# Performance work log

Measured on AMD Instinct MI355X. Metric: run time of the kernel, lower is better.

## Reference

```python
import jax, jax.numpy as jnp
import numpy as np

GROUP_SIZE = 32

def setup_inputs() -> dict:
    key = jax.random.key(0)
    k_x, k_w, k_b, k_se, k_zp = jax.random.split(key, 5)
    B, S, IN_CH, OUT_CH = 4, 2048, 4096, 4096
    n_groups = IN_CH // GROUP_SIZE
    x = jax.random.normal(k_x, (B, S, IN_CH), dtype=jnp.float32)
    weight = jax.random.normal(k_w, (OUT_CH, IN_CH), dtype=jnp.float32) * 0.02
    bias = jax.random.normal(k_b, (OUT_CH,), dtype=jnp.float32)
    # po2 scale: 2**e with int8 exponent; pick exponents so scale ~ weight magnitude / 15
    exp = jax.random.randint(k_se, (OUT_CH, n_groups, 1), -10, -6).astype(jnp.float32)
    weight_scale = jnp.exp2(exp)  # float32
    weight_zp = jax.random.randint(k_zp, (OUT_CH, n_groups, 1), 0, 16).astype(jnp.float32)
    return {"x": x, "weight": weight, "bias": bias,
            "weight_scale": weight_scale, "weight_zp": weight_zp}

def reference(x, weight, bias, weight_scale, weight_zp):
    out_ch, in_ch = weight.shape
    # [O, n_groups, group_size]
    w_g = weight.reshape(out_ch, in_ch // GROUP_SIZE, GROUP_SIZE)
    # asym uint4 quantize: clamp(round(w/scale + zp), 0, 15)
    q = jnp.clip(jnp.round(w_g / weight_scale + weight_zp), 0.0, 15.0)
    # dequantize: (q - zp) * scale, flatten groups back to [O, I]
    dq = ((q - weight_zp) * weight_scale).reshape(out_ch, in_ch)
    # F.linear: x @ dq.T + bias
    return jnp.einsum('bsi,oi->bso', x, dq) + bias
```

## Files before the change

### kernel.cpp

```cpp
#include <hip/hip_runtime.h>
#include <hip/hip_bf16.h>
#include <stdint.h>

typedef unsigned short ushort_t;
typedef __bf16 bf16x8 __attribute__((ext_vector_type(8)));
typedef float f32x4 __attribute__((ext_vector_type(4)));


__device__ __forceinline__ ushort_t f2bf(float f) {
  unsigned int u = __float_as_uint(f);
  u += 0x7FFFu + ((u >> 16) & 1u);
  return (ushort_t)(u >> 16);
}

typedef __attribute__((address_space(1))) void gvoid_t;
typedef __attribute__((address_space(3))) void lvoid_t;

__device__ __forceinline__ void async_cp16(const ushort_t* g, ushort_t* l) {
  __builtin_amdgcn_global_load_lds((gvoid_t*)g, (lvoid_t*)l, 16, 0, 0);
}


__global__ __launch_bounds__(256) void cvt_x_kernel(const float4* __restrict__ x,
                                                    ushort4* __restrict__ xb, int n4) {
  int i = blockIdx.x * blockDim.x + threadIdx.x;
  if (i >= n4) return;
  float4 v = x[i];
  ushort4 o;
  o.x = f2bf(v.x); o.y = f2bf(v.y); o.z = f2bf(v.z); o.w = f2bf(v.w);
  xb[i] = o;
}


__device__ __forceinline__ float dq1(float w, float rs, float s, float z) {
  float q = rintf(w * rs + z);
  q = fminf(fmaxf(q, 0.0f), 15.0f);
  return (q - z) * s;
}

__global__ __launch_bounds__(256) void dequant_w_kernel(const float* __restrict__ w,
                                                        const float* __restrict__ sc,
                                                        const float* __restrict__ zp,
                                                        ushort_t* __restrict__ wq,
                                                        int total) {
  int base = (blockIdx.x * blockDim.x + threadIdx.x) * 8;
  if (base >= total) return;
  int gi = base >> 5;
  float s = sc[gi], z = zp[gi];
  float rs = 1.0f / s;
  const float4* w4 = (const float4*)(w + base);
  float4 a = w4[0], b = w4[1];
  ushort4 o0, o1;
  o0.x = f2bf(dq1(a.x, rs, s, z)); o0.y = f2bf(dq1(a.y, rs, s, z));
  o0.z = f2bf(dq1(a.z, rs, s, z)); o0.w = f2bf(dq1(a.w, rs, s, z));
  o1.x = f2bf(dq1(b.x, rs, s, z)); o1.y = f2bf(dq1(b.y, rs, s, z));
  o1.z = f2bf(dq1(b.z, rs, s, z)); o1.w = f2bf(dq1(b.w, rs, s, z));
  ushort4* out4 = (ushort4*)(wq + base);
  out4[0] = o0; out4[1] = o1;
}


#define BM 128
#define BN 128
#define BK 64

__global__ __launch_bounds__(256) void gemm_bt_bias_kernel(
    const ushort_t* __restrict__ A,
    const ushort_t* __restrict__ B,
    const float* __restrict__ bias,
    float* __restrict__ C,
    int M, int N, int K) {
  __shared__ ushort_t sA[BM * BK];
  __shared__ ushort_t sB[BN * BK];

  const int tid  = threadIdx.x;
  const int wave = tid >> 6;
  const int lane = tid & 63;
  const int bn = blockIdx.x, bm = blockIdx.y;
  const int m0 = bm * BM, n0 = bn * BN;
  const int wm = (wave >> 1) * 64, wn = (wave & 1) * 64;
  const int l15 = lane & 15, l4 = lane >> 4;

  f32x4 acc[4][4] = {};

  const int srow = tid >> 3;
  const int gcol = ((tid & 7) ^ ((tid >> 3) & 7)) * 8;

  const int xa = l15 & 7;

  for (int k0 = 0; k0 < K; k0 += BK) {
    __syncthreads();
#pragma unroll
    for (int it = 0; it < 4; ++it)
      async_cp16(A + (size_t)(m0 + srow + it * 32) * K + k0 + gcol,
                 &sA[(it * 256 + wave * 64) * 8]);
#pragma unroll
    for (int it = 0; it < 4; ++it)
      async_cp16(B + (size_t)(n0 + srow + it * 32) * K + k0 + gcol,
                 &sB[(it * 256 + wave * 64) * 8]);
    __syncthreads();

#pragma unroll
    for (int kk = 0; kk < BK; kk += 32) {
      bf16x8 af[4], bfr[4];
#pragma unroll
      for (int t = 0; t < 4; ++t) {
        int pc = (((kk >> 3) + l4) ^ xa) << 3;
        af[t] = *(const bf16x8*)&sA[(wm + t * 16 + l15) * BK + pc];
      }
#pragma unroll
      for (int t = 0; t < 4; ++t) {
        int pc = (((kk >> 3) + l4) ^ xa) << 3;
        bfr[t] = *(const bf16x8*)&sB[(wn + t * 16 + l15) * BK + pc];
      }
#pragma unroll
      for (int mt = 0; mt < 4; ++mt)
#pragma unroll
        for (int nt = 0; nt < 4; ++nt)
          acc[mt][nt] = __builtin_amdgcn_mfma_f32_16x16x32_bf16(
              af[mt], bfr[nt], acc[mt][nt], 0, 0, 0);
    }
  }

  const int ccol = n0 + wn + l15;
  const int crow = m0 + wm + l4 * 4;
#pragma unroll
  for (int nt = 0; nt < 4; ++nt) {
    float bv = bias[ccol + nt * 16];
#pragma unroll
    for (int mt = 0; mt < 4; ++mt) {
#pragma unroll
      for (int r = 0; r < 4; ++r)
        C[(size_t)(crow + mt * 16 + r) * N + ccol + nt * 16] = acc[mt][nt][r] + bv;
    }
  }
}


extern "C" void kernel_launch(void* const* d_in, const int* in_sizes, int n_in,
                              void* d_out, int out_size, void* d_ws, size_t ws_size,
                              hipStream_t stream) {
  const float* x    = (const float*)d_in[0];
  const float* w    = (const float*)d_in[1];
  const float* bias = (const float*)d_in[2];
  const float* sc   = (const float*)d_in[3];
  const float* zp   = (const float*)d_in[4];
  float* out = (float*)d_out;

  const int N = in_sizes[2];
  const int K = in_sizes[1] / N;
  const int M = in_sizes[0] / K;

  ushort_t* xb = (ushort_t*)d_ws;
  ushort_t* wq = xb + (size_t)M * K;

  int n4 = (M * K) / 4;
  cvt_x_kernel<<<(n4 + 255) / 256, 256, 0, stream>>>((const float4*)x, (ushort4*)xb, n4);

  int wthreads = (N * K) / 8;
  dequant_w_kernel<<<(wthreads + 255) / 256, 256, 0, stream>>>(w, sc, zp, wq, N * K);

  dim3 grid(N / BN, M / BM);
  gemm_bt_bias_kernel<<<grid, 256, 0, stream>>>(xb, wq, bias, out, M, N, K);
}
```

Baseline: 595.6 us.

## Use 256x256 double-buffered GEMM tiles with interleaved staging and XCD-aware block remap

The GEMM moves from 128x128 single-buffered tiles with 4 waves to 256x256 tiles with 8 waves and a double-buffered LDS. Each k-step is split into quarters that interleave async global-to-LDS copies for the next tile with MFMA work, using explicit barriers, vmcnt waits and s_setprio. A 1D grid with a remap across groups of 8 is meant to improve L2 locality across XCDs. The conversion kernels now write 16-byte vectors. The larger tiles raise register and LDS pressure and leave fewer blocks in the grid (512).

```diff
diff --git a/kernel.cpp b/kernel.cpp
--- a/kernel.cpp
+++ b/kernel.cpp
@@ -5,6 +5,7 @@
 typedef unsigned short ushort_t;
 typedef __bf16 bf16x8 __attribute__((ext_vector_type(8)));
 typedef float f32x4 __attribute__((ext_vector_type(4)));
+typedef ushort_t ushort8v __attribute__((ext_vector_type(8)));
 
 
 __device__ __forceinline__ ushort_t f2bf(float f) {
@@ -22,12 +23,13 @@
 
 
 __global__ __launch_bounds__(256) void cvt_x_kernel(const float4* __restrict__ x,
-                                                    ushort4* __restrict__ xb, int n4) {
-  int i = blockIdx.x * blockDim.x + threadIdx.x;
-  if (i >= n4) return;
-  float4 v = x[i];
-  ushort4 o;
-  o.x = f2bf(v.x); o.y = f2bf(v.y); o.z = f2bf(v.z); o.w = f2bf(v.w);
+                                                    ushort8v* __restrict__ xb, int n8) {
+  int i = blockIdx.x * 256 + threadIdx.x;
+  if (i >= n8) return;
+  float4 a = x[2 * i], b = x[2 * i + 1];
+  ushort8v o;
+  o[0] = f2bf(a.x); o[1] = f2bf(a.y); o[2] = f2bf(a.z); o[3] = f2bf(a.w);
+  o[4] = f2bf(b.x); o[5] = f2bf(b.y); o[6] = f2bf(b.z); o[7] = f2bf(b.w);
   xb[i] = o;
 }
 
@@ -41,98 +43,165 @@
 __global__ __launch_bounds__(256) void dequant_w_kernel(const float* __restrict__ w,
                                                         const float* __restrict__ sc,
                                                         const float* __restrict__ zp,
-                                                        ushort_t* __restrict__ wq,
-                                                        int total) {
-  int base = (blockIdx.x * blockDim.x + threadIdx.x) * 8;
-  if (base >= total) return;
+                                                        ushort8v* __restrict__ wq, int n8) {
+  int i = blockIdx.x * 256 + threadIdx.x;
+  if (i >= n8) return;
+  int base = i * 8;
   int gi = base >> 5;
   float s = sc[gi], z = zp[gi];
   float rs = 1.0f / s;
   const float4* w4 = (const float4*)(w + base);
   float4 a = w4[0], b = w4[1];
-  ushort4 o0, o1;
-  o0.x = f2bf(dq1(a.x, rs, s, z)); o0.y = f2bf(dq1(a.y, rs, s, z));
-  o0.z = f2bf(dq1(a.z, rs, s, z)); o0.w = f2bf(dq1(a.w, rs, s, z));
-  o1.x = f2bf(dq1(b.x, rs, s, z)); o1.y = f2bf(dq1(b.y, rs, s, z));
-  o1.z = f2bf(dq1(b.z, rs, s, z)); o1.w = f2bf(dq1(b.w, rs, s, z));
-  ushort4* out4 = (ushort4*)(wq + base);
-  out4[0] = o0; out4[1] = o1;
-}
-
-
-#define BM 128
-#define BN 128
+  ushort8v o;
+  o[0] = f2bf(dq1(a.x, rs, s, z)); o[1] = f2bf(dq1(a.y, rs, s, z));
+  o[2] = f2bf(dq1(a.z, rs, s, z)); o[3] = f2bf(dq1(a.w, rs, s, z));
+  o[4] = f2bf(dq1(b.x, rs, s, z)); o[5] = f2bf(dq1(b.y, rs, s, z));
+  o[6] = f2bf(dq1(b.z, rs, s, z)); o[7] = f2bf(dq1(b.w, rs, s, z));
+  wq[i] = o;
+}
+
+
+#define BM 256
+#define BN 256
 #define BK 64
 
-__global__ __launch_bounds__(256) void gemm_bt_bias_kernel(
+__device__ __forceinline__ f32x4 mfma16(bf16x8 a, bf16x8 b, f32x4 c) {
+  return __builtin_amdgcn_mfma_f32_16x16x32_bf16(a, b, c, 0, 0, 0);
+}
+
+template <int MH, int NHB>
+__device__ __forceinline__ void mfma_quad(f32x4 acc[2][4][4], const bf16x8 Afr[4][2],
+                                          const bf16x8 Bfr[4][2]) {
+#pragma unroll
+  for (int k = 0; k < 2; ++k)
+#pragma unroll
+    for (int mt = 0; mt < 4; ++mt)
+#pragma unroll
+      for (int nt = 0; nt < 2; ++nt)
+        acc[MH][mt][NHB * 2 + nt] =
+            mfma16(Afr[mt][k], Bfr[NHB * 2 + nt][k], acc[MH][mt][NHB * 2 + nt]);
+}
+
+__global__ __launch_bounds__(512, 2) void gemm_bt_bias_kernel(
     const ushort_t* __restrict__ A,
     const ushort_t* __restrict__ B,
     const float* __restrict__ bias,
     float* __restrict__ C,
     int M, int N, int K) {
-  __shared__ ushort_t sA[BM * BK];
-  __shared__ ushort_t sB[BN * BK];
+  __shared__ ushort_t sA[2][BM * BK];
+  __shared__ ushort_t sB[2][BN * BK];
 
   const int tid  = threadIdx.x;
   const int wave = tid >> 6;
   const int lane = tid & 63;
-  const int bn = blockIdx.x, bm = blockIdx.y;
-  const int m0 = bm * BM, n0 = bn * BN;
-  const int wm = (wave >> 1) * 64, wn = (wave & 1) * 64;
   const int l15 = lane & 15, l4 = lane >> 4;
 
-  f32x4 acc[4][4] = {};
+  int wg = blockIdx.x;
+  const int nwg = gridDim.x;
+  if ((nwg & 7) == 0) wg = (wg & 7) * (nwg >> 3) + (wg >> 3);
+  const int nbn = N / BN;
+  const int m0 = (wg / nbn) * BM, n0 = (wg % nbn) * BN;
+  const int wm = (wave >> 2) * 128, wn = (wave & 3) * 64;
 
   const int srow = tid >> 3;
-  const int gcol = ((tid & 7) ^ ((tid >> 3) & 7)) * 8;
-
-  const int xa = l15 & 7;
-
-  for (int k0 = 0; k0 < K; k0 += BK) {
-    __syncthreads();
-#pragma unroll
-    for (int it = 0; it < 4; ++it)
-      async_cp16(A + (size_t)(m0 + srow + it * 32) * K + k0 + gcol,
-                 &sA[(it * 256 + wave * 64) * 8]);
-#pragma unroll
-    for (int it = 0; it < 4; ++it)
-      async_cp16(B + (size_t)(n0 + srow + it * 32) * K + k0 + gcol,
-                 &sB[(it * 256 + wave * 64) * 8]);
-    __syncthreads();
-
-#pragma unroll
-    for (int kk = 0; kk < BK; kk += 32) {
-      bf16x8 af[4], bfr[4];
-#pragma unroll
-      for (int t = 0; t < 4; ++t) {
-        int pc = (((kk >> 3) + l4) ^ xa) << 3;
-        af[t] = *(const bf16x8*)&sA[(wm + t * 16 + l15) * BK + pc];
-      }
-#pragma unroll
-      for (int t = 0; t < 4; ++t) {
-        int pc = (((kk >> 3) + l4) ^ xa) << 3;
-        bfr[t] = *(const bf16x8*)&sB[(wn + t * 16 + l15) * BK + pc];
-      }
-#pragma unroll
-      for (int mt = 0; mt < 4; ++mt)
-#pragma unroll
-        for (int nt = 0; nt < 4; ++nt)
-          acc[mt][nt] = __builtin_amdgcn_mfma_f32_16x16x32_bf16(
-              af[mt], bfr[nt], acc[mt][nt], 0, 0, 0);
-    }
+  const int scol = ((tid & 7) ^ (srow & 7)) * 8;
+  const int ldst = wave * 64 * 8;
+
+  const int xa  = l15 & 7;
+  const int pc0 = (l4 ^ xa) << 3;
+  const int pc1 = ((4 + l4) ^ xa) << 3;
+  const int aoff = (wm + l15) * BK;
+  const int boff = (wn + l15) * BK;
+
+  f32x4 acc[2][4][4] = {};
+  bf16x8 Afr[4][2], Bfr[4][2];
+
+#define STAGE_A(sb, s, kn) \
+  async_cp16(A + (size_t)(m0 + (s) * 64 + srow) * K + (kn) + scol, &sA[sb][(s) * 4096 + ldst])
+#define STAGE_B(sb, s, kn) \
+  async_cp16(B + (size_t)(n0 + (s) * 64 + srow) * K + (kn) + scol, &sB[sb][(s) * 4096 + ldst])
+#define LDA(rb, mh, mt, k) \
+  (*(const bf16x8*)&sA[rb][aoff + ((mh) * 64 + (mt) * 16) * BK + ((k) ? pc1 : pc0)])
+#define LDB(rb, nt, k) \
+  (*(const bf16x8*)&sB[rb][boff + (nt) * 16 * BK + ((k) ? pc1 : pc0)])
+#define BAR()   __builtin_amdgcn_s_barrier()
+#define LGKM0() asm volatile("s_waitcnt lgkmcnt(0)" ::: "memory")
+#define VM(n)   asm volatile("s_waitcnt vmcnt(" #n ")" ::: "memory")
+#define PRIO(p) __builtin_amdgcn_s_setprio(p)
+
+  STAGE_B(0, 0, 0); STAGE_B(0, 1, 0); STAGE_A(0, 0, 0);
+  STAGE_B(0, 2, 0); STAGE_B(0, 3, 0); STAGE_A(0, 2, 0);
+  STAGE_A(0, 1, 0); STAGE_A(0, 3, 0);
+  VM(2);
+  BAR();
+
+  const int nK = K / BK;
+#pragma unroll 2
+  for (int t = 0; t < nK - 1; ++t) {
+    const int rb = t & 1, sb = rb ^ 1;
+    const int kn = (t + 1) * BK;
+#pragma unroll
+    for (int mt = 0; mt < 4; ++mt) { Afr[mt][0] = LDA(rb, 0, mt, 0); Afr[mt][1] = LDA(rb, 0, mt, 1); }
+#pragma unroll
+    for (int nt = 0; nt < 2; ++nt) { Bfr[nt][0] = LDB(rb, nt, 0); Bfr[nt][1] = LDB(rb, nt, 1); }
+    STAGE_B(sb, 0, kn); STAGE_B(sb, 1, kn); STAGE_A(sb, 0, kn);
+    BAR(); LGKM0();
+    PRIO(1); mfma_quad<0, 0>(acc, Afr, Bfr); PRIO(0);
+    BAR();
+#pragma unroll
+    for (int nt = 2; nt < 4; ++nt) { Bfr[nt][0] = LDB(rb, nt, 0); Bfr[nt][1] = LDB(rb, nt, 1); }
+    STAGE_B(sb, 2, kn); STAGE_B(sb, 3, kn); STAGE_A(sb, 2, kn);
+    BAR(); LGKM0();
+    PRIO(1); mfma_quad<0, 1>(acc, Afr, Bfr); PRIO(0);
+    VM(6);
+    BAR();
+#pragma unroll
+    for (int mt = 0; mt < 4; ++mt) { Afr[mt][0] = LDA(rb, 1, mt, 0); Afr[mt][1] = LDA(rb, 1, mt, 1); }
+    STAGE_A(sb, 1, kn); STAGE_A(sb, 3, kn);
+    BAR(); LGKM0();
+    PRIO(1); mfma_quad<1, 0>(acc, Afr, Bfr); PRIO(0);
+    BAR();
+    PRIO(1); mfma_quad<1, 1>(acc, Afr, Bfr); PRIO(0);
+    VM(2);
+    BAR();
+  }
+
+  {
+    const int rb = (nK - 1) & 1;
+#pragma unroll
+    for (int mt = 0; mt < 4; ++mt) { Afr[mt][0] = LDA(rb, 0, mt, 0); Afr[mt][1] = LDA(rb, 0, mt, 1); }
+#pragma unroll
+    for (int nt = 0; nt < 2; ++nt) { Bfr[nt][0] = LDB(rb, nt, 0); Bfr[nt][1] = LDB(rb, nt, 1); }
+    BAR(); LGKM0();
+    PRIO(1); mfma_quad<0, 0>(acc, Afr, Bfr); PRIO(0);
+    BAR();
+#pragma unroll
+    for (int nt = 2; nt < 4; ++nt) { Bfr[nt][0] = LDB(rb, nt, 0); Bfr[nt][1] = LDB(rb, nt, 1); }
+    BAR(); LGKM0();
+    PRIO(1); mfma_quad<0, 1>(acc, Afr, Bfr); PRIO(0);
+    VM(0);
+    BAR();
+#pragma unroll
+    for (int mt = 0; mt < 4; ++mt) { Afr[mt][0] = LDA(rb, 1, mt, 0); Afr[mt][1] = LDA(rb, 1, mt, 1); }
+    BAR(); LGKM0();
+    PRIO(1); mfma_quad<1, 0>(acc, Afr, Bfr); PRIO(0);
+    BAR();
+    PRIO(1); mfma_quad<1, 1>(acc, Afr, Bfr); PRIO(0);
   }
 
   const int ccol = n0 + wn + l15;
   const int crow = m0 + wm + l4 * 4;
 #pragma unroll
   for (int nt = 0; nt < 4; ++nt) {
-    float bv = bias[ccol + nt * 16];
-#pragma unroll
-    for (int mt = 0; mt < 4; ++mt) {
-#pragma unroll
-      for (int r = 0; r < 4; ++r)
-        C[(size_t)(crow + mt * 16 + r) * N + ccol + nt * 16] = acc[mt][nt][r] + bv;
-    }
+    const float bv = bias[ccol + nt * 16];
+#pragma unroll
+    for (int mh = 0; mh < 2; ++mh)
+#pragma unroll
+      for (int mt = 0; mt < 4; ++mt)
+#pragma unroll
+        for (int r = 0; r < 4; ++r)
+          C[(size_t)(crow + mh * 64 + mt * 16 + r) * N + ccol + nt * 16] =
+              acc[mh][mt][nt][r] + bv;
   }
 }
 
@@ -154,12 +223,12 @@
   ushort_t* xb = (ushort_t*)d_ws;
   ushort_t* wq = xb + (size_t)M * K;
 
-  int n4 = (M * K) / 4;
-  cvt_x_kernel<<<(n4 + 255) / 256, 256, 0, stream>>>((const float4*)x, (ushort4*)xb, n4);
-
-  int wthreads = (N * K) / 8;
-  dequant_w_kernel<<<(wthreads + 255) / 256, 256, 0, stream>>>(w, sc, zp, wq, N * K);
-
-  dim3 grid(N / BN, M / BM);
-  gemm_bt_bias_kernel<<<grid, 256, 0, stream>>>(xb, wq, bias, out, M, N, K);
-}
+  int xn8 = (M * K) / 8;
+  cvt_x_kernel<<<(xn8 + 255) / 256, 256, 0, stream>>>((const float4*)x, (ushort8v*)xb, xn8);
+
+  int wn8 = (N * K) / 8;
+  dequant_w_kernel<<<(wn8 + 255) / 256, 256, 0, stream>>>(w, sc, zp, (ushort8v*)wq, wn8);
+
+  dim3 grid((M / BM) * (N / BN));
+  gemm_bt_bias_kernel<<<grid, 512, 0, stream>>>(xb, wq, bias, out, M, N, K);
+}
```

Result: faster. 539.4 us (-9.4%).
